# Kernel optimization log

Measured on AMD Instinct MI355X. Metric: run time of the kernel, lower is better.

The kernel has to match this reference:

```python
import jax, jax.numpy as jnp
import numpy as np

B, N, D = 1, 4096, 320
HEADS, DIM_HEAD = 8, 40
PHASE, Hm, Wm = 3, 64, 64  # guidance mask spatial dims; Hm*Wm == N


def setup_inputs() -> dict:
    key = jax.random.key(0)
    ks = jax.random.split(key, 7)
    s = 0.02
    x = jax.random.normal(ks[0], (B, N, D), jnp.float32)
    guidance_mask = jax.random.bernoulli(ks[1], 0.25, (B, PHASE, Hm, Wm)).astype(jnp.float32)
    Wq = jax.random.normal(ks[2], (D, HEADS * DIM_HEAD), jnp.float32) * s
    Wk = jax.random.normal(ks[3], (D, HEADS * DIM_HEAD), jnp.float32) * s
    Wv = jax.random.normal(ks[4], (D, HEADS * DIM_HEAD), jnp.float32) * s
    Wo = jax.random.normal(ks[5], (HEADS * DIM_HEAD, D), jnp.float32) * s
    bo = jnp.zeros((D,), jnp.float32)
    return {"x": x, "guidance_mask": guidance_mask, "Wq": Wq, "Wk": Wk,
            "Wv": Wv, "Wo": Wo, "bo": bo}


def reference(x, guidance_mask, Wq, Wk, Wv, Wo, bo):
    b, n, _ = x.shape
    h, dh = HEADS, DIM_HEAD
    scale = dh ** (-0.5)

    def split_heads(t):
        # b n (h d) -> (b h) n d
        return t.reshape(b, n, h, dh).transpose(0, 2, 1, 3).reshape(b * h, n, dh)

    q = split_heads(x @ Wq)
    k = split_heads(x @ Wk)
    v = split_heads(x @ Wv)

    sim = jnp.einsum('bid,bjd->bij', q, k) * scale  # (b*h, n, n)

    _, p, Hh, Ww = guidance_mask.shape
    HW = Hh * Ww  # == n
    g = guidance_mask.reshape(b, p, HW)
    # sum over phases of outer products, clamped at 1 (binary block mask)
    mask_sim = jnp.minimum(jnp.einsum('bpi,bpj->bij', g, g), 1.0)  # (b, HW, HW)
    mask_sim = jnp.repeat(mask_sim, h, axis=0)  # (b*h, HW, HW), heads within each b

    neg = -jnp.finfo(sim.dtype).max
    # original: sim[:, :, :HW][mask_sim == 0] = -max ; here n == HW so full matrix
    sim = jnp.where(mask_sim == 0, neg, sim)

    attn = jax.nn.softmax(sim, axis=-1)
    out = jnp.einsum('bij,bjd->bid', attn, v)  # (b*h, n, dh)
    out = out.reshape(b, h, n, dh).transpose(0, 2, 1, 3).reshape(b, n, h * dh)
    return out @ Wo + bo
```

## Files before the change

### kernel.cpp

```cpp
#include <hip/hip_runtime.h>
#include <hip/hip_bf16.h>
#include <stdint.h>

#define NT 4096
#define DM 320
#define NH 8
#define DH 40
#define KS 4
#define QSCALE 0.22811013f
#define PSTR 68
#define KFJB 640

typedef float f32x4 __attribute__((ext_vector_type(4)));
typedef __bf16 bf16x8 __attribute__((ext_vector_type(8)));

__device__ __forceinline__ unsigned short f2b(float f) {
  unsigned u = __builtin_bit_cast(unsigned, f);
  u += 0x7FFFu + ((u >> 16) & 1u);
  return (unsigned short)(u >> 16);
}

__device__ __forceinline__ bf16x8 ld_bf8(const unsigned short* p) {
  uint4 v = *(const uint4*)p;
  return __builtin_bit_cast(bf16x8, v);
}

__device__ __forceinline__ f32x4 mfma16(bf16x8 a, bf16x8 b, f32x4 c) {
  return __builtin_amdgcn_mfma_f32_16x16x32_bf16(a, b, c, 0, 0, 0);
}

__device__ __forceinline__ float fexp2(float x) {
#if __has_builtin(__builtin_amdgcn_exp2f)
  return __builtin_amdgcn_exp2f(x);
#else
  float r; asm("v_exp_f32 %0, %1" : "=v"(r) : "v"(x)); return r;
#endif
}

__device__ __forceinline__ uint2 pack4(float a, float b, float c, float d) {
  uint2 pk;
  pk.x = (unsigned)f2b(a) | ((unsigned)f2b(b) << 16);
  pk.y = (unsigned)f2b(c) | ((unsigned)f2b(d) << 16);
  return pk;
}

__device__ __forceinline__ uint4 idfrag(int idx) {
  uint4 r;
  r.x = (idx == 0 ? 0x3F80u : 0u) | (idx == 1 ? 0x3F800000u : 0u);
  r.y = (idx == 2 ? 0x3F80u : 0u) | (idx == 3 ? 0x3F800000u : 0u);
  r.z = (idx == 4 ? 0x3F80u : 0u) | (idx == 5 ? 0x3F800000u : 0u);
  r.w = (idx == 6 ? 0x3F80u : 0u) | (idx == 7 ? 0x3F800000u : 0u);
  return r;
}

__device__ __forceinline__ size_t fmi(int tile, int nk, int k, int o) {
  return ((size_t)tile * nk + (k >> 5)) * 512 + (size_t)((k >> 3) & 3) * 128 +
         (size_t)(o & 15) * 8 + (k & 7);
}

__global__ __launch_bounds__(256) void prep_kernel(
    const float* __restrict__ x, const float* __restrict__ g,
    const float* __restrict__ Wq, const float* __restrict__ Wk,
    const float* __restrict__ Wv, const float* __restrict__ Wo,
    unsigned short* __restrict__ xbf, unsigned char* __restrict__ sgp,
    unsigned short* __restrict__ Wtf, int* __restrict__ perm,
    int* __restrict__ invp, int* __restrict__ nqp,
    unsigned char* __restrict__ tsig) {
  const int b = blockIdx.x, t = threadIdx.x;
  if (b == 100) {
    __shared__ unsigned long long sa[256], sb[256];
    unsigned char mys[16];
    unsigned long long ca = 0ull, cb = 0ull;
#pragma unroll
    for (int i = 0; i < 16; ++i) {
      int tok = t * 16 + i;
      unsigned s = 0;
      if (g[tok] != 0.f)          s |= 1u;
      if (g[NT + tok] != 0.f)     s |= 2u;
      if (g[2 * NT + tok] != 0.f) s |= 4u;
      mys[i] = (unsigned char)s;
      if (s < 4) ca += 1ull << (16 * s);
      else       cb += 1ull << (16 * (s - 4));
    }
    sa[t] = ca; sb[t] = cb;
    __syncthreads();
    for (int off = 1; off < 256; off <<= 1) {
      unsigned long long va = (t >= off) ? sa[t - off] : 0ull;
      unsigned long long vb = (t >= off) ? sb[t - off] : 0ull;
      __syncthreads();
      sa[t] += va; sb[t] += vb;
      __syncthreads();
    }
    const unsigned long long ta = sa[255], tb = sb[255];
    const int t1 = (int)((ta >> 16) & 0xffff), t2 = (int)((ta >> 32) & 0xffff),
              t3 = (int)((ta >> 48) & 0xffff), t4 = (int)(tb & 0xffff),
              t5 = (int)((tb >> 16) & 0xffff), t6 = (int)((tb >> 32) & 0xffff),
              t7 = (int)((tb >> 48) & 0xffff);
    const int b1 = 0, b2 = t1, b3 = b2 + t2, b4 = b3 + t3, b5 = b4 + t4,
              b6 = b5 + t5, b7 = b6 + t6, b0 = b7 + t7;
    unsigned long long ra = sa[t] - ca;
    unsigned long long rb = sb[t] - cb;
    ra += ((unsigned long long)(unsigned)b0)        |
          ((unsigned long long)(unsigned)b1 << 16)  |
          ((unsigned long long)(unsigned)b2 << 32)  |
          ((unsigned long long)(unsigned)b3 << 48);
    rb += ((unsigned long long)(unsigned)b4)        |
          ((unsigned long long)(unsigned)b5 << 16)  |
          ((unsigned long long)(unsigned)b6 << 32)  |
          ((unsigned long long)(unsigned)b7 << 48);
#pragma unroll
    for (int i = 0; i < 16; ++i) {
      int tok = t * 16 + i;
      unsigned s = mys[i];
      int sh = 16 * (int)(s & 3u);
      int p;
      if (s < 4) { p = (int)((ra >> sh) & 0xffff); ra += 1ull << sh; }
      else       { p = (int)((rb >> sh) & 0xffff); rb += 1ull << sh; }
      perm[p] = tok; invp[tok] = p; sgp[p] = (unsigned char)s;
    }
    if (t == 0) nqp[0] = b0;
    if (t < 64) {
      const int lo = t * 64, hi = lo + 64;
      unsigned o = 0;
      if (b1 < hi && b2 > lo && b2 > b1) o |= 1u;
      if (b2 < hi && b3 > lo && b3 > b2) o |= 2u;
      if (b3 < hi && b4 > lo && b4 > b3) o |= 3u;
      if (b4 < hi && b5 > lo && b5 > b4) o |= 4u;
      if (b5 < hi && b6 > lo && b6 > b5) o |= 5u;
      if (b6 < hi && b7 > lo && b7 > b6) o |= 6u;
      if (b7 < hi && b0 > lo && b0 > b7) o |= 7u;
      tsig[t] = (unsigned char)o;
    }
    return;
  }
  if (b > 100) {
    int base = (b - 101) * 2560;
#pragma unroll
    for (int j = 0; j < 10; ++j) {
      int i = (base + j * 256 + t) * 4;
      int m = i / DM, k = i % DM;
      float4 v = *(const float4*)(x + i);
      ushort4 u;
      u.x = f2b(v.x); u.y = f2b(v.y); u.z = f2b(v.z); u.w = f2b(v.w);
      *(ushort4*)(xbf + fmi(m >> 4, 10, k, m)) = u;
    }
    return;
  }
  __shared__ __align__(16) unsigned short lt[64 * 72];
  int kx = b % 5, cy = b / 5;
  int cm = cy % 5;
  const float* src;
  int rowbase;
  if (cy < 5)       { src = Wq; rowbase = cm * 64; }
  else if (cy < 10) { src = Wk; rowbase = 320 + cm * 64; }
  else if (cy < 15) { src = Wv; rowbase = 640 + cm * 64; }
  else              { src = Wo; rowbase = 960 + cm * 64; }
  const int c0 = cm * 64;
  const int k0 = kx * 64;
#pragma unroll
  for (int i = 0; i < 4; ++i) {
    int kr = (t >> 4) + i * 16, cc = (t & 15) * 4;
    float4 w4 = *(const float4*)&src[(size_t)(k0 + kr) * DM + c0 + cc];
    lt[(cc + 0) * 72 + kr] = f2b(w4.x);
    lt[(cc + 1) * 72 + kr] = f2b(w4.y);
    lt[(cc + 2) * 72 + kr] = f2b(w4.z);
    lt[(cc + 3) * 72 + kr] = f2b(w4.w);
  }
  __syncthreads();
#pragma unroll
  for (int i = 0; i < 2; ++i) {
    int idx = t + i * 256, cl = idx >> 3, ch = idx & 7;
    int c = rowbase + cl, k = k0 + ch * 8;
    *(uint4*)&Wtf[fmi(c >> 4, 10, k, c)] = *(const uint4*)&lt[cl * 72 + ch * 8];
  }
}

__global__ __launch_bounds__(256, 4) void qkv_gemm(
    const unsigned short* __restrict__ xbf, const unsigned short* __restrict__ Wtf,
    const int* __restrict__ invp,
    unsigned short* __restrict__ Qb, unsigned short* __restrict__ Kf,
    unsigned short* __restrict__ Vk) {
  const int t = threadIdx.x;
  const int w = t >> 6, lane = t & 63, quad = lane >> 4, ln = lane & 15;
  const int m0 = blockIdx.x * 64;
  const int cy = blockIdx.y;
  const int a = cy / 5;
  const int cc0 = (cy % 5) * 64;
  const int mt = (m0 >> 4) + w;
  const int ct0 = a * 20 + (cc0 >> 4);

  f32x4 acc[4] = {{0,0,0,0},{0,0,0,0},{0,0,0,0},{0,0,0,0}};
  for (int kc = 0; kc < 10; ++kc) {
    bf16x8 xf = ld_bf8(xbf + ((size_t)(mt * 10 + kc)) * 512 + lane * 8);
#pragma unroll
    for (int nt = 0; nt < 4; ++nt) {
      bf16x8 wf = ld_bf8(Wtf + ((size_t)((ct0 + nt) * 10 + kc)) * 512 + lane * 8);
      acc[nt] = mfma16(wf, xf, acc[nt]);
    }
  }
  const int bp = invp[m0 + w * 16 + ln];
  if (a == 0) {
#pragma unroll
    for (int nt = 0; nt < 4; ++nt) {
      int c = cc0 + nt * 16 + quad * 4;
      int h = c / DH, d = c % DH;
      uint2 pk = pack4(acc[nt][0] * QSCALE, acc[nt][1] * QSCALE,
                       acc[nt][2] * QSCALE, acc[nt][3] * QSCALE);
      *(uint2*)&Qb[((size_t)h * NT + bp) * 64 + d] = pk;
    }
  } else {
    unsigned short* dst = (a == 1) ? Kf : Vk;
#pragma unroll
    for (int nt = 0; nt < 4; ++nt) {
      int c = cc0 + nt * 16 + quad * 4;
      int h = c / DH, d = c % DH;
      uint2 pk = pack4(acc[nt][0], acc[nt][1], acc[nt][2], acc[nt][3]);
      size_t base = ((size_t)h * 256 + (bp >> 4)) * KFJB;
      size_t idx = (d < 32)
          ? base + (size_t)(d >> 3) * 128 + (size_t)(bp & 15) * 8 + (d & 7)
          : base + 512 + (size_t)(bp & 15) * 8 + (d - 32);
      *(uint2*)&dst[idx] = pk;
    }
  }
}

__global__ __launch_bounds__(256) void retile_kernel(
    const unsigned short* __restrict__ Vk, unsigned short* __restrict__ Vf) {
  const int t = threadIdx.x;
  const int w = t >> 6, lane = t & 63, ln = lane & 15, jg = lane >> 4;
  const bf16x8 b1f = __builtin_bit_cast(bf16x8, idfrag(ln - jg * 8));
  const bf16x8 b2f = __builtin_bit_cast(bf16x8, idfrag(ln + 16 - jg * 8));
  const uint4 z4 = {0, 0, 0, 0};
#pragma unroll
  for (int i = 0; i < 4; ++i) {
    const int task = (blockIdx.x * 4 + w) * 4 + i;
    const int h = task >> 8, jb = task & 255;
    const unsigned short* kb = Vk + ((size_t)h * 256 + jb) * KFJB;
    uint4 f0 = *(const uint4*)(kb + lane * 8);
    uint4 f1 = z4;
    if (lane < 16) f1 = *(const uint4*)(kb + 512 + lane * 8);
    f32x4 d1 = {0,0,0,0}, d2 = {0,0,0,0}, d3 = {0,0,0,0};
    d1 = mfma16(__builtin_bit_cast(bf16x8, f0), b1f, d1);
    d2 = mfma16(__builtin_bit_cast(bf16x8, f0), b2f, d2);
    d3 = mfma16(__builtin_bit_cast(bf16x8, f1), b1f, d3);
    const int bp = jb * 16 + jg * 4;
#pragma unroll
    for (int ot = 0; ot < 3; ++ot) {
      int dd = ot * 16 + ln;
      if (ot == 2 && ln >= 8) continue;
      f32x4 dv = (ot == 0) ? d1 : (ot == 1) ? d2 : d3;
      size_t idx = ((((((size_t)(h * 64 + (bp >> 6)) * 3 + (dd >> 4)) * 2 +
                       ((bp >> 5) & 1)) * 4 + ((bp >> 3) & 3)) * 16 + (dd & 15))) * 8 +
                   (bp & 7);
      *(uint2*)&Vf[idx] = pack4(dv[0], dv[1], dv[2], dv[3]);
    }
  }
}

__global__ __launch_bounds__(256, 4) void attn_kernel(
    const unsigned short* __restrict__ Qb, const unsigned short* __restrict__ Kf,
    const unsigned short* __restrict__ Vf, const unsigned char* __restrict__ sgp,
    const int* __restrict__ nqp, const unsigned char* __restrict__ tsg,
    unsigned short* __restrict__ Opf, float* __restrict__ Lpart,
    unsigned short* __restrict__ Ubf) {
  __shared__ __align__(16) unsigned short pt[4][32 * PSTR];
  __shared__ float vs[4][48];
  const int t = threadIdx.x;
  const int w = t >> 6, lane = t & 63, quad = lane >> 4, ln = lane & 15;
  const int h = blockIdx.y, sp = blockIdx.z;
  const int nq = nqp[0];
  const int nkt = (nq + 63) >> 6;
  const int nq_pad = (nq + 127) & ~127;

  const unsigned short* Vfh = Vf + (size_t)h * 196608;
  const uint4 z4 = {0, 0, 0, 0};
  const uint4 ones4 = {0x3F803F80u, 0x3F803F80u, 0x3F803F80u, 0x3F803F80u};
  const bf16x8 onesb = __builtin_bit_cast(bf16x8, ones4);

  if (blockIdx.x == 32) {
    if (sp != 0) return;
    f32x4 o[3] = {{0,0,0,0},{0,0,0,0},{0,0,0,0}};
    for (int jt = w; jt < 64; jt += 4) {
#pragma unroll
      for (int ot = 0; ot < 3; ++ot) {
        uint4 v0 = *(const uint4*)(Vfh + ((size_t)((jt * 3 + ot) * 2 + 0)) * 512 +
                                   lane * 8);
        uint4 v1 = *(const uint4*)(Vfh + ((size_t)((jt * 3 + ot) * 2 + 1)) * 512 +
                                   lane * 8);
        o[ot] = mfma16(__builtin_bit_cast(bf16x8, v0), onesb, o[ot]);
        o[ot] = mfma16(__builtin_bit_cast(bf16x8, v1), onesb, o[ot]);
      }
    }
    if (ln == 0) {
#pragma unroll
      for (int ot = 0; ot < 3; ++ot)
#pragma unroll
        for (int r = 0; r < 4; ++r) vs[w][ot * 16 + quad * 4 + r] = o[ot][r];
    }
    __syncthreads();
    if (t < DH) {
      float s = vs[0][t] + vs[1][t] + vs[2][t] + vs[3][t];
      Ubf[h * DH + t] = f2b(s * (1.0f / (float)NT));
    }
    return;
  }

  const int qt = (blockIdx.x + 8 * sp) & 31;
  if (qt * 128 >= nq_pad) return;
  const int qrow = qt * 128 + w * 32;

  unsigned qv = *(const unsigned*)(sgp + qrow)      | *(const unsigned*)(sgp + qrow + 4)
              | *(const unsigned*)(sgp + qrow + 8)  | *(const unsigned*)(sgp + qrow + 12)
              | *(const unsigned*)(sgp + qrow + 16) | *(const unsigned*)(sgp + qrow + 20)
              | *(const unsigned*)(sgp + qrow + 24) | *(const unsigned*)(sgp + qrow + 28);
  qv |= qv >> 16; qv |= qv >> 8;
  const unsigned qor = qv & 255u;

  const unsigned short* Kfh = Kf + (size_t)h * 256 * KFJB;
  unsigned short* ptw = pt[w];
  const bool vone = (ln == 8);

  bf16x8 qa[2][2];
  unsigned sqx4[2];
  f32x4 o[3][2] = {{{0,0,0,0},{0,0,0,0}},{{0,0,0,0},{0,0,0,0}},{{0,0,0,0},{0,0,0,0}}};

#pragma unroll
  for (int tq = 0; tq < 2; ++tq) {
    int bp = qrow + tq * 16 + ln;
    const unsigned short* Qp = Qb + ((size_t)h * NT + bp) * 64;
    qa[tq][0] = ld_bf8(Qp + quad * 8);
    uint4 q1 = z4;
    if (quad == 0) q1 = *(const uint4*)(Qp + 32);
    qa[tq][1] = __builtin_bit_cast(bf16x8, q1);
    sqx4[tq] = (unsigned)sgp[bp] * 0x01010101u;
  }

  for (int jt = sp; jt < nkt; jt += KS) {
    if ((tsg[jt] & qor) == 0) continue;
    uint4 kfr0[4], kfr1[4];
#pragma unroll
    for (int nt = 0; nt < 4; ++nt) {
      const unsigned short* kb = Kfh + (size_t)(jt * 4 + nt) * KFJB;
      kfr0[nt] = *(const uint4*)(kb + lane * 8);
      kfr1[nt] = z4;
      if (lane < 16) kfr1[nt] = *(const uint4*)(kb + 512 + lane * 8);
    }
#pragma unroll
    for (int nt = 0; nt < 4; ++nt) {
      bf16x8 ka0 = __builtin_bit_cast(bf16x8, kfr0[nt]);
      bf16x8 ka1 = __builtin_bit_cast(bf16x8, kfr1[nt]);
      unsigned spj = *(const unsigned*)(sgp + jt * 64 + nt * 16 + quad * 4);
#pragma unroll
      for (int tq = 0; tq < 2; ++tq) {
        f32x4 acc = {0.f, 0.f, 0.f, 0.f};
        acc = mfma16(ka0, qa[tq][0], acc);
        acc = mfma16(ka1, qa[tq][1], acc);
        unsigned m4 = spj & sqx4[tq];
        unsigned u[4];
#pragma unroll
        for (int r = 0; r < 4; ++r) {
          unsigned mb = (m4 >> (8 * r)) & 255u;
          float am = mb ? acc[r] : -3.0e38f;
          u[r] = __builtin_bit_cast(unsigned, fexp2(am));
        }
        uint2 pk;
        pk.x = (u[0] >> 16) | (u[1] & 0xffff0000u);
        pk.y = (u[2] >> 16) | (u[3] & 0xffff0000u);
        *(uint2*)&ptw[(tq * 16 + ln) * PSTR + nt * 16 + quad * 4] = pk;
      }
    }
    uint4 vfr[6];
#pragma unroll
    for (int ot = 0; ot < 3; ++ot)
#pragma unroll
      for (int c = 0; c < 2; ++c)
        vfr[ot * 2 + c] =
            *(const uint4*)(Vfh + ((size_t)((jt * 3 + ot) * 2 + c)) * 512 + lane * 8);
    if (vone) { vfr[4] = ones4; vfr[5] = ones4; }

    bf16x8 pb[2][2];
    asm volatile("s_waitcnt lgkmcnt(0)" ::: "memory");
#pragma unroll
    for (int tq = 0; tq < 2; ++tq) {
      pb[tq][0] = ld_bf8(&ptw[(tq * 16 + ln) * PSTR + quad * 8]);
      pb[tq][1] = ld_bf8(&ptw[(tq * 16 + ln) * PSTR + 32 + quad * 8]);
    }
#pragma unroll
    for (int ot = 0; ot < 3; ++ot) {
      bf16x8 va0 = __builtin_bit_cast(bf16x8, vfr[ot * 2]);
      bf16x8 va1 = __builtin_bit_cast(bf16x8, vfr[ot * 2 + 1]);
#pragma unroll
      for (int tq = 0; tq < 2; ++tq) {
        o[ot][tq] = mfma16(va0, pb[tq][0], o[ot][tq]);
        o[ot][tq] = mfma16(va1, pb[tq][1], o[ot][tq]);
      }
    }
  }

#pragma unroll
  for (int tq = 0; tq < 2; ++tq) {
    int bp = qrow + tq * 16 + ln;
#pragma unroll
    for (int ot = 0; ot < 3; ++ot) {
      int d0 = ot * 16 + quad * 4;
      if (d0 < DH) {
        int c = h * DH + d0;
        uint2 pk = pack4(o[ot][tq][0], o[ot][tq][1], o[ot][tq][2], o[ot][tq][3]);
        *(uint2*)&Opf[fmi(sp * 256 + (bp >> 4), 10, c, bp)] = pk;
      }
    }
    if (quad == 2)
      Lpart[sp * NT + bp] = o[2][tq][0];
  }
}

__global__ __launch_bounds__(256, 4) void combine_kernel(
    const unsigned short* __restrict__ Opf, const float* __restrict__ Lpart,
    const int* __restrict__ perm, const int* __restrict__ nqp,
    unsigned short* __restrict__ Abf) {
  const int t = threadIdx.x;
  const int w = t >> 6, lane = t & 63;
  const int task = blockIdx.x * 4 + w;
  const int tile = task / 10, kc = task % 10;
  const int nq_pad = (nqp[0] + 127) & ~127;
  if (tile * 16 >= nq_pad) return;
  const int row = tile * 16 + (lane & 15);

  float L = 0.f;
#pragma unroll
  for (int sp = 0; sp < KS; ++sp) L += Lpart[sp * NT + row];
  const float inv = 1.f / L;

  float s8[8] = {0, 0, 0, 0, 0, 0, 0, 0};
#pragma unroll
  for (int sp = 0; sp < KS; ++sp) {
    uint4 v = *(const uint4*)(Opf + ((size_t)((sp * 256 + tile) * 10 + kc)) * 512 +
                              lane * 8);
    unsigned vv[4] = {v.x, v.y, v.z, v.w};
#pragma unroll
    for (int j = 0; j < 4; ++j) {
      s8[2 * j]     += __builtin_bit_cast(float, vv[j] << 16);
      s8[2 * j + 1] += __builtin_bit_cast(float, vv[j] & 0xffff0000u);
    }
  }
  uint4 av;
  av.x = (unsigned)f2b(s8[0] * inv) | ((unsigned)f2b(s8[1] * inv) << 16);
  av.y = (unsigned)f2b(s8[2] * inv) | ((unsigned)f2b(s8[3] * inv) << 16);
  av.z = (unsigned)f2b(s8[4] * inv) | ((unsigned)f2b(s8[5] * inv) << 16);
  av.w = (unsigned)f2b(s8[6] * inv) | ((unsigned)f2b(s8[7] * inv) << 16);
  const int m = perm[row];
  *(uint4*)&Abf[fmi(m >> 4, 10, kc * 32 + (lane >> 4) * 8, m)] = av;
}

__global__ __launch_bounds__(256, 4) void out_gemm(
    const unsigned short* __restrict__ Abf, const unsigned short* __restrict__ Wtf,
    const float* __restrict__ bo, const int* __restrict__ invp,
    const int* __restrict__ nqp, const unsigned short* __restrict__ Ubf,
    float* __restrict__ out) {
  const int t = threadIdx.x;
  const int w = t >> 6, lane = t & 63, quad = lane >> 4, ln = lane & 15;
  const int m0 = blockIdx.x * 64;
  const int cc0 = blockIdx.y * 64;
  const int mt = (m0 >> 4) + w;
  const int m = m0 + w * 16 + ln;
  const int ct0 = 60 + (cc0 >> 4);
  const bool uni = invp[m] >= nqp[0];

  f32x4 acc[4] = {{0,0,0,0},{0,0,0,0},{0,0,0,0},{0,0,0,0}};
  for (int kc = 0; kc < 10; ++kc) {
    uint4 uv = *(const uint4*)(Ubf + kc * 32 + quad * 8);
    uint4 av = *(const uint4*)(Abf + ((size_t)(mt * 10 + kc)) * 512 + lane * 8);
    if (uni) av = uv;
    bf16x8 af = __builtin_bit_cast(bf16x8, av);
#pragma unroll
    for (int nt = 0; nt < 4; ++nt) {
      bf16x8 wf = ld_bf8(Wtf + ((size_t)((ct0 + nt) * 10 + kc)) * 512 + lane * 8);
      acc[nt] = mfma16(wf, af, acc[nt]);
    }
  }
#pragma unroll
  for (int nt = 0; nt < 4; ++nt) {
    int c = cc0 + nt * 16 + quad * 4;
    float4 bv = *(const float4*)(bo + c);
    float4 ov;
    ov.x = acc[nt][0] + bv.x;
    ov.y = acc[nt][1] + bv.y;
    ov.z = acc[nt][2] + bv.z;
    ov.w = acc[nt][3] + bv.w;
    *(float4*)(out + (size_t)m * DM + c) = ov;
  }
}

extern "C" void kernel_launch(void* const* d_in, const int* in_sizes, int n_in,
                              void* d_out, int out_size, void* d_ws, size_t ws_size,
                              hipStream_t stream) {
  const float* x  = (const float*)d_in[0];
  const float* g  = (const float*)d_in[1];
  const float* Wq = (const float*)d_in[2];
  const float* Wk = (const float*)d_in[3];
  const float* Wv = (const float*)d_in[4];
  const float* Wo = (const float*)d_in[5];
  const float* bo = (const float*)d_in[6];
  float* out = (float*)d_out;

  char* ws = (char*)d_ws;
  const size_t SGP_OFF  = 0;
  const size_t NQ_OFF   = 4096;
  const size_t TSIG_OFF = 4224;
  const size_t PERM_OFF = 8192;
  const size_t INV_OFF  = 24576;
  const size_t XBF_OFF  = 40960;
  const size_t WTF_OFF = XBF_OFF + (size_t)NT * DM * 2;
  const size_t QB_OFF  = WTF_OFF + (size_t)1280 * DM * 2;
  const size_t KF_OFF  = QB_OFF + (size_t)NH * NT * 64 * 2;
  const size_t VK_OFF  = KF_OFF + (size_t)NH * 256 * KFJB * 2;
  const size_t VF_OFF  = VK_OFF + (size_t)NH * 256 * KFJB * 2;
  const size_t OPF_OFF = VF_OFF + (size_t)NH * 196608 * 2;
  const size_t LP_OFF  = OPF_OFF + (size_t)KS * 256 * 10 * 512 * 2;
  const size_t UBF_OFF = LP_OFF + (size_t)KS * NT * 4;
  const size_t ABF_OFF = UBF_OFF + 4096;
  unsigned char* sgp   = (unsigned char*)(ws + SGP_OFF);
  int* nqp             = (int*)(ws + NQ_OFF);
  unsigned char* tsig  = (unsigned char*)(ws + TSIG_OFF);
  int* perm            = (int*)(ws + PERM_OFF);
  int* invp            = (int*)(ws + INV_OFF);
  unsigned short* xbf  = (unsigned short*)(ws + XBF_OFF);
  unsigned short* Wtf  = (unsigned short*)(ws + WTF_OFF);
  unsigned short* Qb   = (unsigned short*)(ws + QB_OFF);
  unsigned short* Kf   = (unsigned short*)(ws + KF_OFF);
  unsigned short* Vk   = (unsigned short*)(ws + VK_OFF);
  unsigned short* Vf   = (unsigned short*)(ws + VF_OFF);
  unsigned short* Opf  = (unsigned short*)(ws + OPF_OFF);
  float* Lpart         = (float*)(ws + LP_OFF);
  unsigned short* Ubf  = (unsigned short*)(ws + UBF_OFF);
  unsigned short* Abf  = (unsigned short*)(ws + ABF_OFF);

  prep_kernel<<<229, 256, 0, stream>>>(x, g, Wq, Wk, Wv, Wo, xbf, sgp, Wtf,
                                       perm, invp, nqp, tsig);
  qkv_gemm<<<dim3(64, 15), 256, 0, stream>>>(xbf, Wtf, invp, Qb, Kf, Vk);
  retile_kernel<<<128, 256, 0, stream>>>(Vk, Vf);
  attn_kernel<<<dim3(33, NH, KS), 256, 0, stream>>>(Qb, Kf, Vf, sgp, nqp, tsig,
                                                    Opf, Lpart, Ubf);
  combine_kernel<<<640, 256, 0, stream>>>(Opf, Lpart, perm, nqp, Abf);
  out_gemm<<<dim3(64, 5), 256, 0, stream>>>(Abf, Wtf, bo, invp, nqp, Ubf, out);
}
```

Before: 131.5 us.

## Permute x before QKV GEMM, write V tiles directly, skip masked Q/K rows

The bf16 conversion of x moves into a separate kernel that scatters rows into the permuted token order, so the QKV GEMM no longer needs invp. The V projection swaps its MFMA operands and writes the transposed attention tile layout directly, which removes the retile kernel and the intermediate Vk buffer. Q/K blocks beyond the padded count of query-relevant tokens now exit early. The attention split count KS drops from 4 to 2, which halves partial outputs and combine work but gives attention fewer blocks in parallel.

```diff
diff --git a/kernel.cpp b/kernel.cpp
--- a/kernel.cpp
+++ b/kernel.cpp
@@ -6,7 +6,7 @@
 #define DM 320
 #define NH 8
 #define DH 40
-#define KS 4
+#define KS 2
 #define QSCALE 0.22811013f
 #define PSTR 68
 #define KFJB 640
@@ -44,27 +44,17 @@
   return pk;
 }
 
-__device__ __forceinline__ uint4 idfrag(int idx) {
-  uint4 r;
-  r.x = (idx == 0 ? 0x3F80u : 0u) | (idx == 1 ? 0x3F800000u : 0u);
-  r.y = (idx == 2 ? 0x3F80u : 0u) | (idx == 3 ? 0x3F800000u : 0u);
-  r.z = (idx == 4 ? 0x3F80u : 0u) | (idx == 5 ? 0x3F800000u : 0u);
-  r.w = (idx == 6 ? 0x3F80u : 0u) | (idx == 7 ? 0x3F800000u : 0u);
-  return r;
-}
-
 __device__ __forceinline__ size_t fmi(int tile, int nk, int k, int o) {
   return ((size_t)tile * nk + (k >> 5)) * 512 + (size_t)((k >> 3) & 3) * 128 +
          (size_t)(o & 15) * 8 + (k & 7);
 }
 
-__global__ __launch_bounds__(256) void prep_kernel(
-    const float* __restrict__ x, const float* __restrict__ g,
+__global__ __launch_bounds__(256) void prep0_kernel(
+    const float* __restrict__ g,
     const float* __restrict__ Wq, const float* __restrict__ Wk,
     const float* __restrict__ Wv, const float* __restrict__ Wo,
-    unsigned short* __restrict__ xbf, unsigned char* __restrict__ sgp,
-    unsigned short* __restrict__ Wtf, int* __restrict__ perm,
-    int* __restrict__ invp, int* __restrict__ nqp,
+    unsigned char* __restrict__ sgp, unsigned short* __restrict__ Wtf,
+    int* __restrict__ perm, int* __restrict__ invp, int* __restrict__ nqp,
     unsigned char* __restrict__ tsig) {
   const int b = blockIdx.x, t = threadIdx.x;
   if (b == 100) {
@@ -133,19 +123,6 @@
     }
     return;
   }
-  if (b > 100) {
-    int base = (b - 101) * 2560;
-#pragma unroll
-    for (int j = 0; j < 10; ++j) {
-      int i = (base + j * 256 + t) * 4;
-      int m = i / DM, k = i % DM;
-      float4 v = *(const float4*)(x + i);
-      ushort4 u;
-      u.x = f2b(v.x); u.y = f2b(v.y); u.z = f2b(v.z); u.w = f2b(v.w);
-      *(ushort4*)(xbf + fmi(m >> 4, 10, k, m)) = u;
-    }
-    return;
-  }
   __shared__ __align__(16) unsigned short lt[64 * 72];
   int kx = b % 5, cy = b / 5;
   int cm = cy % 5;
@@ -175,16 +152,34 @@
   }
 }
 
+__global__ __launch_bounds__(256) void xsort_kernel(
+    const float* __restrict__ x, const int* __restrict__ invp,
+    unsigned short* __restrict__ xbf) {
+  const int t = threadIdx.x;
+  const int base = blockIdx.x * 2560;
+#pragma unroll
+  for (int j = 0; j < 10; ++j) {
+    int i = (base + j * 256 + t) * 4;
+    int m = i / DM, k = i % DM;
+    int bp = invp[m];
+    float4 v = *(const float4*)(x + i);
+    ushort4 u;
+    u.x = f2b(v.x); u.y = f2b(v.y); u.z = f2b(v.z); u.w = f2b(v.w);
+    *(ushort4*)(xbf + fmi(bp >> 4, 10, k, bp)) = u;
+  }
+}
+
 __global__ __launch_bounds__(256, 4) void qkv_gemm(
     const unsigned short* __restrict__ xbf, const unsigned short* __restrict__ Wtf,
-    const int* __restrict__ invp,
+    const int* __restrict__ nqp,
     unsigned short* __restrict__ Qb, unsigned short* __restrict__ Kf,
-    unsigned short* __restrict__ Vk) {
+    unsigned short* __restrict__ Vf) {
   const int t = threadIdx.x;
   const int w = t >> 6, lane = t & 63, quad = lane >> 4, ln = lane & 15;
   const int m0 = blockIdx.x * 64;
   const int cy = blockIdx.y;
   const int a = cy / 5;
+  if (a < 2 && m0 >= ((nqp[0] + 127) & ~127)) return;
   const int cc0 = (cy % 5) * 64;
   const int mt = (m0 >> 4) + w;
   const int ct0 = a * 20 + (cc0 >> 4);
@@ -195,11 +190,12 @@
 #pragma unroll
     for (int nt = 0; nt < 4; ++nt) {
       bf16x8 wf = ld_bf8(Wtf + ((size_t)((ct0 + nt) * 10 + kc)) * 512 + lane * 8);
-      acc[nt] = mfma16(wf, xf, acc[nt]);
-    }
-  }
-  const int bp = invp[m0 + w * 16 + ln];
+      if (a < 2) acc[nt] = mfma16(wf, xf, acc[nt]);
+      else       acc[nt] = mfma16(xf, wf, acc[nt]);
+    }
+  }
   if (a == 0) {
+    const int bp = m0 + w * 16 + ln;
 #pragma unroll
     for (int nt = 0; nt < 4; ++nt) {
       int c = cc0 + nt * 16 + quad * 4;
@@ -208,8 +204,8 @@
                        acc[nt][2] * QSCALE, acc[nt][3] * QSCALE);
       *(uint2*)&Qb[((size_t)h * NT + bp) * 64 + d] = pk;
     }
-  } else {
-    unsigned short* dst = (a == 1) ? Kf : Vk;
+  } else if (a == 1) {
+    const int bp = m0 + w * 16 + ln;
 #pragma unroll
     for (int nt = 0; nt < 4; ++nt) {
       int c = cc0 + nt * 16 + quad * 4;
@@ -219,40 +215,18 @@
       size_t idx = (d < 32)
           ? base + (size_t)(d >> 3) * 128 + (size_t)(bp & 15) * 8 + (d & 7)
           : base + 512 + (size_t)(bp & 15) * 8 + (d - 32);
-      *(uint2*)&dst[idx] = pk;
-    }
-  }
-}
-
-__global__ __launch_bounds__(256) void retile_kernel(
-    const unsigned short* __restrict__ Vk, unsigned short* __restrict__ Vf) {
-  const int t = threadIdx.x;
-  const int w = t >> 6, lane = t & 63, ln = lane & 15, jg = lane >> 4;
-  const bf16x8 b1f = __builtin_bit_cast(bf16x8, idfrag(ln - jg * 8));
-  const bf16x8 b2f = __builtin_bit_cast(bf16x8, idfrag(ln + 16 - jg * 8));
-  const uint4 z4 = {0, 0, 0, 0};
-#pragma unroll
-  for (int i = 0; i < 4; ++i) {
-    const int task = (blockIdx.x * 4 + w) * 4 + i;
-    const int h = task >> 8, jb = task & 255;
-    const unsigned short* kb = Vk + ((size_t)h * 256 + jb) * KFJB;
-    uint4 f0 = *(const uint4*)(kb + lane * 8);
-    uint4 f1 = z4;
-    if (lane < 16) f1 = *(const uint4*)(kb + 512 + lane * 8);
-    f32x4 d1 = {0,0,0,0}, d2 = {0,0,0,0}, d3 = {0,0,0,0};
-    d1 = mfma16(__builtin_bit_cast(bf16x8, f0), b1f, d1);
-    d2 = mfma16(__builtin_bit_cast(bf16x8, f0), b2f, d2);
-    d3 = mfma16(__builtin_bit_cast(bf16x8, f1), b1f, d3);
-    const int bp = jb * 16 + jg * 4;
-#pragma unroll
-    for (int ot = 0; ot < 3; ++ot) {
-      int dd = ot * 16 + ln;
-      if (ot == 2 && ln >= 8) continue;
-      f32x4 dv = (ot == 0) ? d1 : (ot == 1) ? d2 : d3;
-      size_t idx = ((((((size_t)(h * 64 + (bp >> 6)) * 3 + (dd >> 4)) * 2 +
-                       ((bp >> 5) & 1)) * 4 + ((bp >> 3) & 3)) * 16 + (dd & 15))) * 8 +
-                   (bp & 7);
-      *(uint2*)&Vf[idx] = pack4(dv[0], dv[1], dv[2], dv[3]);
+      *(uint2*)&Kf[idx] = pk;
+    }
+  } else {
+    const int bp4 = m0 + w * 16 + quad * 4;
+#pragma unroll
+    for (int nt = 0; nt < 4; ++nt) {
+      int c = cc0 + nt * 16 + ln;
+      int h = c / DH, d = c % DH;
+      size_t idx = ((((((size_t)(h * 64 + (bp4 >> 6)) * 3 + (d >> 4)) * 2 +
+                       ((bp4 >> 5) & 1)) * 4 + ((bp4 >> 3) & 3)) * 16 + (d & 15))) * 8 +
+                   (bp4 & 7);
+      *(uint2*)&Vf[idx] = pack4(acc[nt][0], acc[nt][1], acc[nt][2], acc[nt][3]);
     }
   }
 }
@@ -513,8 +487,7 @@
   const size_t WTF_OFF = XBF_OFF + (size_t)NT * DM * 2;
   const size_t QB_OFF  = WTF_OFF + (size_t)1280 * DM * 2;
   const size_t KF_OFF  = QB_OFF + (size_t)NH * NT * 64 * 2;
-  const size_t VK_OFF  = KF_OFF + (size_t)NH * 256 * KFJB * 2;
-  const size_t VF_OFF  = VK_OFF + (size_t)NH * 256 * KFJB * 2;
+  const size_t VF_OFF  = KF_OFF + (size_t)NH * 256 * KFJB * 2;
   const size_t OPF_OFF = VF_OFF + (size_t)NH * 196608 * 2;
   const size_t LP_OFF  = OPF_OFF + (size_t)KS * 256 * 10 * 512 * 2;
   const size_t UBF_OFF = LP_OFF + (size_t)KS * NT * 4;
@@ -528,17 +501,16 @@
   unsigned short* Wtf  = (unsigned short*)(ws + WTF_OFF);
   unsigned short* Qb   = (unsigned short*)(ws + QB_OFF);
   unsigned short* Kf   = (unsigned short*)(ws + KF_OFF);
-  unsigned short* Vk   = (unsigned short*)(ws + VK_OFF);
   unsigned short* Vf   = (unsigned short*)(ws + VF_OFF);
   unsigned short* Opf  = (unsigned short*)(ws + OPF_OFF);
   float* Lpart         = (float*)(ws + LP_OFF);
   unsigned short* Ubf  = (unsigned short*)(ws + UBF_OFF);
   unsigned short* Abf  = (unsigned short*)(ws + ABF_OFF);
 
-  prep_kernel<<<229, 256, 0, stream>>>(x, g, Wq, Wk, Wv, Wo, xbf, sgp, Wtf,
-                                       perm, invp, nqp, tsig);
-  qkv_gemm<<<dim3(64, 15), 256, 0, stream>>>(xbf, Wtf, invp, Qb, Kf, Vk);
-  retile_kernel<<<128, 256, 0, stream>>>(Vk, Vf);
+  prep0_kernel<<<101, 256, 0, stream>>>(g, Wq, Wk, Wv, Wo, sgp, Wtf,
+                                        perm, invp, nqp, tsig);
+  xsort_kernel<<<128, 256, 0, stream>>>(x, invp, xbf);
+  qkv_gemm<<<dim3(64, 15), 256, 0, stream>>>(xbf, Wtf, nqp, Qb, Kf, Vf);
   attn_kernel<<<dim3(33, NH, KS), 256, 0, stream>>>(Qb, Kf, Vf, sgp, nqp, tsig,
                                                     Opf, Lpart, Ubf);
   combine_kernel<<<640, 256, 0, stream>>>(Opf, Lpart, perm, nqp, Abf);
```

After: 138.5 us. 5.3% more time.

## Fuse split-K combine into attention via intra-block wave reduction

Applied to the files above, without the earlier changes.

The attention kernel now gives each block a 32-row query tile and splits the key tiles across its four waves, reducing their partial outputs and row sums through shared memory. Wave 0 then normalizes and writes the permuted bf16 result straight to Abf. This removes the separate combine kernel and the global round-trip of partial outputs and Lpart. In exchange it uses more shared memory (about 18KB of reduction buffers), which may lower occupancy, and it adds a block-wide barrier with a serial reduction on one wave.

```diff
diff --git a/kernel.cpp b/kernel.cpp
--- a/kernel.cpp
+++ b/kernel.cpp
@@ -6,7 +6,6 @@
 #define DM 320
 #define NH 8
 #define DH 40
-#define KS 4
 #define QSCALE 0.22811013f
 #define PSTR 68
 #define KFJB 640
@@ -260,14 +259,16 @@
 __global__ __launch_bounds__(256, 4) void attn_kernel(
     const unsigned short* __restrict__ Qb, const unsigned short* __restrict__ Kf,
     const unsigned short* __restrict__ Vf, const unsigned char* __restrict__ sgp,
-    const int* __restrict__ nqp, const unsigned char* __restrict__ tsg,
-    unsigned short* __restrict__ Opf, float* __restrict__ Lpart,
-    unsigned short* __restrict__ Ubf) {
+    const int* __restrict__ perm, const int* __restrict__ nqp,
+    const unsigned char* __restrict__ tsg,
+    unsigned short* __restrict__ Abf, unsigned short* __restrict__ Ubf) {
   __shared__ __align__(16) unsigned short pt[4][32 * PSTR];
+  __shared__ float red[3][24][64];
   __shared__ float vs[4][48];
+  __shared__ __align__(16) unsigned short ob[32][40];
   const int t = threadIdx.x;
   const int w = t >> 6, lane = t & 63, quad = lane >> 4, ln = lane & 15;
-  const int h = blockIdx.y, sp = blockIdx.z;
+  const int h = blockIdx.y;
   const int nq = nqp[0];
   const int nkt = (nq + 63) >> 6;
   const int nq_pad = (nq + 127) & ~127;
@@ -277,8 +278,7 @@
   const uint4 ones4 = {0x3F803F80u, 0x3F803F80u, 0x3F803F80u, 0x3F803F80u};
   const bf16x8 onesb = __builtin_bit_cast(bf16x8, ones4);
 
-  if (blockIdx.x == 32) {
-    if (sp != 0) return;
+  if (blockIdx.x == 128) {
     f32x4 o[3] = {{0,0,0,0},{0,0,0,0},{0,0,0,0}};
     for (int jt = w; jt < 64; jt += 4) {
 #pragma unroll
@@ -305,9 +305,9 @@
     return;
   }
 
-  const int qt = (blockIdx.x + 8 * sp) & 31;
-  if (qt * 128 >= nq_pad) return;
-  const int qrow = qt * 128 + w * 32;
+  const int qt32 = blockIdx.x;
+  if (qt32 * 32 >= nq_pad) return;
+  const int qrow = qt32 * 32;
 
   unsigned qv = *(const unsigned*)(sgp + qrow)      | *(const unsigned*)(sgp + qrow + 4)
               | *(const unsigned*)(sgp + qrow + 8)  | *(const unsigned*)(sgp + qrow + 12)
@@ -335,7 +335,7 @@
     sqx4[tq] = (unsigned)sgp[bp] * 0x01010101u;
   }
 
-  for (int jt = sp; jt < nkt; jt += KS) {
+  for (int jt = w; jt < nkt; jt += 4) {
     if ((tsg[jt] & qor) == 0) continue;
     uint4 kfr0[4], kfr1[4];
 #pragma unroll
@@ -397,59 +397,55 @@
     }
   }
 
-#pragma unroll
-  for (int tq = 0; tq < 2; ++tq) {
-    int bp = qrow + tq * 16 + ln;
-#pragma unroll
-    for (int ot = 0; ot < 3; ++ot) {
-      int d0 = ot * 16 + quad * 4;
-      if (d0 < DH) {
-        int c = h * DH + d0;
-        uint2 pk = pack4(o[ot][tq][0], o[ot][tq][1], o[ot][tq][2], o[ot][tq][3]);
-        *(uint2*)&Opf[fmi(sp * 256 + (bp >> 4), 10, c, bp)] = pk;
+  if (w) {
+#pragma unroll
+    for (int ot = 0; ot < 3; ++ot)
+#pragma unroll
+      for (int tq = 0; tq < 2; ++tq)
+#pragma unroll
+        for (int r = 0; r < 4; ++r)
+          red[w - 1][ot * 8 + tq * 4 + r][lane] = o[ot][tq][r];
+  }
+  __syncthreads();
+  if (w == 0) {
+#pragma unroll
+    for (int ot = 0; ot < 3; ++ot)
+#pragma unroll
+      for (int tq = 0; tq < 2; ++tq)
+#pragma unroll
+        for (int r = 0; r < 4; ++r) {
+          float s = o[ot][tq][r];
+          s += red[0][ot * 8 + tq * 4 + r][lane];
+          s += red[1][ot * 8 + tq * 4 + r][lane];
+          s += red[2][ot * 8 + tq * 4 + r][lane];
+          o[ot][tq][r] = s;
+        }
+#pragma unroll
+    for (int tq = 0; tq < 2; ++tq) {
+      float Lb = __shfl(o[2][tq][0], 32 + ln, 64);
+      float inv = 1.f / Lb;
+#pragma unroll
+      for (int ot = 0; ot < 3; ++ot) {
+        int d0 = ot * 16 + quad * 4;
+        if (d0 < DH) {
+          uint2 pk = pack4(o[ot][tq][0] * inv, o[ot][tq][1] * inv,
+                           o[ot][tq][2] * inv, o[ot][tq][3] * inv);
+          *(uint2*)&ob[tq * 16 + ln][d0] = pk;
+        }
       }
     }
-    if (quad == 2)
-      Lpart[sp * NT + bp] = o[2][tq][0];
-  }
-}
-
-__global__ __launch_bounds__(256, 4) void combine_kernel(
-    const unsigned short* __restrict__ Opf, const float* __restrict__ Lpart,
-    const int* __restrict__ perm, const int* __restrict__ nqp,
-    unsigned short* __restrict__ Abf) {
-  const int t = threadIdx.x;
-  const int w = t >> 6, lane = t & 63;
-  const int task = blockIdx.x * 4 + w;
-  const int tile = task / 10, kc = task % 10;
-  const int nq_pad = (nqp[0] + 127) & ~127;
-  if (tile * 16 >= nq_pad) return;
-  const int row = tile * 16 + (lane & 15);
-
-  float L = 0.f;
-#pragma unroll
-  for (int sp = 0; sp < KS; ++sp) L += Lpart[sp * NT + row];
-  const float inv = 1.f / L;
-
-  float s8[8] = {0, 0, 0, 0, 0, 0, 0, 0};
-#pragma unroll
-  for (int sp = 0; sp < KS; ++sp) {
-    uint4 v = *(const uint4*)(Opf + ((size_t)((sp * 256 + tile) * 10 + kc)) * 512 +
-                              lane * 8);
-    unsigned vv[4] = {v.x, v.y, v.z, v.w};
-#pragma unroll
-    for (int j = 0; j < 4; ++j) {
-      s8[2 * j]     += __builtin_bit_cast(float, vv[j] << 16);
-      s8[2 * j + 1] += __builtin_bit_cast(float, vv[j] & 0xffff0000u);
-    }
-  }
-  uint4 av;
-  av.x = (unsigned)f2b(s8[0] * inv) | ((unsigned)f2b(s8[1] * inv) << 16);
-  av.y = (unsigned)f2b(s8[2] * inv) | ((unsigned)f2b(s8[3] * inv) << 16);
-  av.z = (unsigned)f2b(s8[4] * inv) | ((unsigned)f2b(s8[5] * inv) << 16);
-  av.w = (unsigned)f2b(s8[6] * inv) | ((unsigned)f2b(s8[7] * inv) << 16);
-  const int m = perm[row];
-  *(uint4*)&Abf[fmi(m >> 4, 10, kc * 32 + (lane >> 4) * 8, m)] = av;
+    asm volatile("s_waitcnt lgkmcnt(0)" ::: "memory");
+#pragma unroll
+    for (int p = 0; p < 3; ++p) {
+      int idx = p * 64 + lane;
+      if (idx < 160) {
+        int row = idx / 5, cc = idx % 5;
+        int m = perm[qrow + row];
+        uint4 vv = *(const uint4*)&ob[row][cc * 8];
+        *(uint4*)&Abf[fmi(m >> 4, 10, h * DH + cc * 8, m)] = vv;
+      }
+    }
+  }
 }
 
 __global__ __launch_bounds__(256, 4) void out_gemm(
@@ -515,9 +511,7 @@
   const size_t KF_OFF  = QB_OFF + (size_t)NH * NT * 64 * 2;
   const size_t VK_OFF  = KF_OFF + (size_t)NH * 256 * KFJB * 2;
   const size_t VF_OFF  = VK_OFF + (size_t)NH * 256 * KFJB * 2;
-  const size_t OPF_OFF = VF_OFF + (size_t)NH * 196608 * 2;
-  const size_t LP_OFF  = OPF_OFF + (size_t)KS * 256 * 10 * 512 * 2;
-  const size_t UBF_OFF = LP_OFF + (size_t)KS * NT * 4;
+  const size_t UBF_OFF = VF_OFF + (size_t)NH * 196608 * 2;
   const size_t ABF_OFF = UBF_OFF + 4096;
   unsigned char* sgp   = (unsigned char*)(ws + SGP_OFF);
   int* nqp             = (int*)(ws + NQ_OFF);
@@ -530,8 +524,6 @@
   unsigned short* Kf   = (unsigned short*)(ws + KF_OFF);
   unsigned short* Vk   = (unsigned short*)(ws + VK_OFF);
   unsigned short* Vf   = (unsigned short*)(ws + VF_OFF);
-  unsigned short* Opf  = (unsigned short*)(ws + OPF_OFF);
-  float* Lpart         = (float*)(ws + LP_OFF);
   unsigned short* Ubf  = (unsigned short*)(ws + UBF_OFF);
   unsigned short* Abf  = (unsigned short*)(ws + ABF_OFF);
 
@@ -539,8 +531,7 @@
                                        perm, invp, nqp, tsig);
   qkv_gemm<<<dim3(64, 15), 256, 0, stream>>>(xbf, Wtf, invp, Qb, Kf, Vk);
   retile_kernel<<<128, 256, 0, stream>>>(Vk, Vf);
-  attn_kernel<<<dim3(33, NH, KS), 256, 0, stream>>>(Qb, Kf, Vf, sgp, nqp, tsig,
-                                                    Opf, Lpart, Ubf);
-  combine_kernel<<<640, 256, 0, stream>>>(Opf, Lpart, perm, nqp, Abf);
+  attn_kernel<<<dim3(129, NH), 256, 0, stream>>>(Qb, Kf, Vf, sgp, perm, nqp,
+                                                 tsig, Abf, Ubf);
   out_gemm<<<dim3(64, 5), 256, 0, stream>>>(Abf, Wtf, bo, invp, nqp, Ubf, out);
 }
```

Result: faster. 128.2 us (-2.5%).
